# Kernel tuning notes

Hardware: AMD Instinct MI355X
Metric: run time of the kernel (lower is better)

## Reference

```python
import jax, jax.numpy as jnp
import numpy as np

ALPHA = 0.2
NEG = -9e15


def _gru(x, Wih, Whh, bih, bhh):
    # x: [B, T, F]; PyTorch nn.GRU cell equations, scan over time.
    H = Whh.shape[1]
    xg = jnp.einsum('btf,gf->btg', x, Wih) + bih  # [B,T,3H]

    def step(h, gi):
        gh = h @ Whh.T + bhh
        ir, iz, inn = jnp.split(gi, 3, axis=-1)
        hr, hz, hn = jnp.split(gh, 3, axis=-1)
        r = jax.nn.sigmoid(ir + hr)
        z = jax.nn.sigmoid(iz + hz)
        n = jnp.tanh(inn + r * hn)
        h = (1.0 - z) * n + z * h
        return h, h

    h0 = jnp.zeros((x.shape[0], H), x.dtype)
    _, ys = jax.lax.scan(step, h0, jnp.swapaxes(xg, 0, 1))
    return jnp.swapaxes(ys, 0, 1)  # [B,T,H]


def _gru_attn(x, Wih, Whh, bih, bhh, aw, ab):
    out = _gru(x, Wih, Whh, bih, bhh)              # [B,T,H]
    w = jax.nn.softmax(out @ aw + ab, axis=1)       # [B,T,1]
    return jnp.sum(out * w, axis=1)                 # [B,H]


def _gat(h, mask, W, a):
    # GraphAttentionLayer with concat=True: elu(softmax(mask(leakyrelu(Wh1+Wh2^T))) @ Wh)
    Wh = h @ W                                      # [N,O]
    O = W.shape[1]
    e = jax.nn.leaky_relu((Wh @ a[:O]) + (Wh @ a[O:]).T, ALPHA)  # [N,N]
    att = jax.nn.softmax(jnp.where(mask, e, NEG), axis=1)
    return jax.nn.elu(att @ Wh)


def setup_inputs() -> dict:
    key = jax.random.key(0)
    ks = iter(jax.random.split(key, 40))
    B, S, Wk, D, F = 1, 2048, 32, 5, 16
    H, E, NS = 128, 128, 16

    def rn(shape, scale=0.1):
        return jax.random.normal(next(ks), shape, jnp.float32) * scale

    inp = {
        'stock_features': jax.random.normal(next(ks), (B, S, Wk, D, F), jnp.float32),
        'stock_to_sector': jax.random.randint(next(ks), (S,), 0, NS, jnp.int32),
        'inter_adj': jax.random.randint(next(ks), (NS, NS), 0, 2, jnp.int32),
        'gru1_Wih': rn((3 * H, F)), 'gru1_Whh': rn((3 * H, H)),
        'gru1_bih': rn((3 * H,)), 'gru1_bhh': rn((3 * H,)),
        'attn1_w': rn((H, 1)), 'attn1_b': rn((1,)),
        'gat_intra_W': rn((H, E)), 'gat_intra_a': rn((2 * E, 1)),
        'grug_Wih': rn((3 * E, E)), 'grug_Whh': rn((3 * E, E)),
        'grug_bih': rn((3 * E,)), 'grug_bhh': rn((3 * E,)),
        'attng_w': rn((E, 1)), 'attng_b': rn((1,)),
        'grua_Wih': rn((3 * E, H)), 'grua_Whh': rn((3 * E, E)),
        'grua_bih': rn((3 * E,)), 'grua_bhh': rn((3 * E,)),
        'attna_w': rn((E, 1)), 'attna_b': rn((1,)),
        'gat_inter_W': rn((E, E)), 'gat_inter_a': rn((2 * E, 1)),
        'fusion_w': rn((3 * E, E)), 'fusion_b': rn((E,)),
        'ret_w': rn((E, 1)), 'ret_b': rn((1,)),
        'mov_w': rn((E, 1)), 'mov_b': rn((1,)),
    }
    return inp


def reference(stock_features, stock_to_sector, inter_adj,
              gru1_Wih, gru1_Whh, gru1_bih, gru1_bhh, attn1_w, attn1_b,
              gat_intra_W, gat_intra_a,
              grug_Wih, grug_Whh, grug_bih, grug_bhh, attng_w, attng_b,
              grua_Wih, grua_Whh, grua_bih, grua_bhh, attna_w, attna_b,
              gat_inter_W, gat_inter_a,
              fusion_w, fusion_b, ret_w, ret_b, mov_w, mov_b):
    B, S, Wk, D, F = stock_features.shape
    H = gru1_Whh.shape[1]
    E = gat_intra_W.shape[1]
    NS = inter_adj.shape[0]

    # Short-term: GRU-attention over days, vectorized over (batch, stock, week).
    x = stock_features.reshape(B * S * Wk, D, F)
    short = _gru_attn(x, gru1_Wih, gru1_Whh, gru1_bih, gru1_bhh, attn1_w, attn1_b)
    short = short.reshape(B, S, Wk, H)

    # Intra-sector GAT on last-week embeddings; per-sector softmax == block mask.
    same_sector = stock_to_sector[:, None] == stock_to_sector[None, :]  # [S,S]
    last = short[:, :, -1, :]                                            # [B,S,H]
    intra = jax.vmap(lambda h: _gat(h, same_sector, gat_intra_W, gat_intra_a))(last)  # [B,S,E]

    # Long-term GRU-attentions.
    lg = _gru_attn(intra.reshape(B * S, 1, E), grug_Wih, grug_Whh, grug_bih, grug_bhh,
                   attng_w, attng_b).reshape(B, S, E)
    la = _gru_attn(short.reshape(B * S, Wk, H), grua_Wih, grua_Whh, grua_bih, grua_bhh,
                   attna_w, attna_b).reshape(B, S, E)

    # Sector embeddings = mean of stock long-term embeddings per sector.
    def sector_mean(g):
        sums = jax.ops.segment_sum(g, stock_to_sector, num_segments=NS)
        cnt = jax.ops.segment_sum(jnp.ones((g.shape[0], 1), g.dtype),
                                  stock_to_sector, num_segments=NS)
        return sums / jnp.maximum(cnt, 1.0)

    sec = jax.vmap(sector_mean)(lg)                                      # [B,NS,E]
    imask = inter_adj > 0
    sec_out = jax.vmap(lambda h: _gat(h, imask, gat_inter_W, gat_inter_a))(sec)
    sec_ps = sec_out[:, stock_to_sector, :]                               # [B,S,E]

    fused = jnp.concatenate([lg, la, sec_ps], axis=-1) @ fusion_w + fusion_b
    returns = (fused @ ret_w + ret_b)[..., 0]
    moves = jax.nn.sigmoid(fused @ mov_w + mov_b)[..., 0]
    return jnp.stack([returns, moves])  # [2,B,S]
```

## Files before the change

### kernel.cpp

```cpp
#include <hip/hip_runtime.h>
#include <math.h>

#define LRELU_A 0.2f
#define NEGBIG (-9.0e15f)

typedef _Float16 f16;
typedef _Float16 f16x8 __attribute__((ext_vector_type(8)));
typedef _Float16 f16x4 __attribute__((ext_vector_type(4)));
typedef float floatx4 __attribute__((ext_vector_type(4)));

__device__ __forceinline__ float rcpf(float x){ return __builtin_amdgcn_rcpf(x); }
__device__ __forceinline__ float sigm(float x){ return rcpf(1.0f+__expf(-x)); }
__device__ __forceinline__ float gru_fuse(float xr, float xz, float xn_pre, float ghn, float h){
    float Er = __expf(-xr);
    float r  = rcpf(1.0f + Er);
    float En = __expf(2.0f*(xn_pre + r*ghn));
    float Ez = __expf(-xz);
    float Dn = En + 1.0f;
    float num = fmaf(h, Dn, (En - 1.0f)*Ez);
    float den = Dn * (1.0f + Ez);
    return num * rcpf(den);
}
__device__ __forceinline__ f16x8 load_cvt8(const float* __restrict__ p){
    float4 a = *(const float4*)p; float4 b = *(const float4*)(p+4);
    f16x8 r; r[0]=(f16)a.x; r[1]=(f16)a.y; r[2]=(f16)a.z; r[3]=(f16)a.w;
    r[4]=(f16)b.x; r[5]=(f16)b.y; r[6]=(f16)b.z; r[7]=(f16)b.w;
    return r;
}
#define MFMA16(A,B,C) __builtin_amdgcn_mfma_f32_16x16x32_f16((A),(B),(C),0,0,0)

__global__ __launch_bounds__(256) void prep_kernel(
    const float* __restrict__ g1Wih, const float* __restrict__ g1Whh,
    const float* __restrict__ gaWih, const float* __restrict__ gaWhh,
    const float* __restrict__ giW,   const float* __restrict__ fw,
    const float* __restrict__ geW,   const float* __restrict__ ggWih,
    const int* __restrict__ sec,
    f16* __restrict__ Wcat1, f16* __restrict__ WcatA,
    f16* __restrict__ WTp, f16* __restrict__ fwp, f16* __restrict__ gep,
    f16* __restrict__ ggp,
    int* __restrict__ memflat, int* __restrict__ pos,
    int* __restrict__ cnt, int* __restrict__ base)
{
    __shared__ int cs[16], wsc[16];
    const int b = blockIdx.x, tid = threadIdx.x;
    if (b < 160){
        for (int idx = b*256+tid; idx < 512*160; idx += 160*256){
            int r = idx/160, k = idx - r*160;
            float v = 0.0f;
            if (r < 256){ if (k < 32){ if (k < 16) v = g1Wih[r*16+k]; } else v = g1Whh[r*128 + (k-32)]; }
            else if (r < 384){ if (k < 16) v = g1Wih[r*16+k]; }
            else { if (k >= 32) v = g1Whh[(r-128)*128 + (k-32)]; }
            Wcat1[idx] = (f16)v;
        }
    } else if (b < 416){
        for (int idx = (b-160)*256+tid; idx < 512*256; idx += 256*256){
            int r = idx >> 8, k = idx & 255;
            float v = 0.0f;
            if (r < 256){ v = (k < 128) ? gaWih[r*128+k] : gaWhh[r*128 + (k-128)]; }
            else if (r < 384){ if (k < 128) v = gaWih[r*128+k]; }
            else { if (k >= 128) v = gaWhh[(r-128)*128 + (k-128)]; }
            WcatA[idx] = (f16)v;
        }
    } else if (b < 480){
        int idx = (b-416)*256+tid;
        int e=idx&7, lane=(idx>>3)&63, fr=idx>>9;
        int kb=fr&3, jb=fr>>2;
        int k = kb*32 + (lane>>4)*8 + e, col = jb*16 + (lane&15);
        WTp[idx] = (f16)giW[k*128 + col];
    } else if (b < 672){
        int idx = (b-480)*256+tid;
        int e=idx&7, lane=(idx>>3)&63, fr=idx>>9;
        int kb=fr%12, jb=fr/12;
        int k = kb*32 + (lane>>4)*8 + e, col = jb*16 + (lane&15);
        fwp[idx] = (f16)fw[k*128 + col];
    } else if (b < 736){
        int idx = (b-672)*256+tid;
        int e=idx&7, lane=(idx>>3)&63, fr=idx>>9;
        int kb=fr&3, jb=fr>>2;
        int k = kb*32 + (lane>>4)*8 + e, col = jb*16 + (lane&15);
        gep[idx] = (f16)geW[k*128 + col];
    } else if (b < 928){
        int idx = (b-736)*256+tid;
        int e=idx&7, lane=(idx>>3)&63, fr=idx>>9;
        int kb=fr&3, jb=(fr>>2)&7, G=fr>>5;
        int row = G*128 + jb*16 + (lane&15), k = kb*32 + (lane>>4)*8 + e;
        ggp[idx] = (f16)ggWih[row*128 + k];
    } else {
        if (tid < 16) cs[tid] = 0;
        __syncthreads();
        for (int s = tid; s < 2048; s += 256) atomicAdd(&cs[sec[s]], 1);
        __syncthreads();
        if (tid == 0){
            int acc = 0;
            for (int g=0; g<16; g++){ cnt[g]=cs[g]; base[g]=acc; wsc[g]=acc; acc+=cs[g]; }
        }
        __syncthreads();
        for (int s = tid; s < 2048; s += 256){
            int g = sec[s];
            int p = atomicAdd(&wsc[g], 1);
            memflat[p] = s;
            pos[s] = p;
        }
    }
}

__global__ __launch_bounds__(512,2) void gru_short(
    const float* __restrict__ x, const f16* __restrict__ Wcat,
    const float* __restrict__ bih, const float* __restrict__ bhh,
    const float* __restrict__ aw, const float* __restrict__ ab,
    f16* __restrict__ out)
{
    __shared__ __align__(16) f16 xs[5][32][40];
    __shared__ __align__(16) f16 hs[2][32][136];
    __shared__ float scpart[2][8][32];
    const int tid = threadIdx.x, w = tid>>6, lane = tid&63;
    const int c = lane&15, quad = lane>>4;

    { f16x4 z4 = {0,0,0,0};
      f16x4* zx = (f16x4*)&xs[0][0][0];
      for (int i=tid; i<1600; i+=512) zx[i] = z4; }

    const int jrow = w*16 + c;
    f16x8 Ar[5], Az[5], Agi, Agh[4];
#pragma unroll
    for (int kb=0;kb<5;kb++){
        Ar[kb] = *(const f16x8*)&Wcat[(size_t)(jrow)*160 + kb*32 + quad*8];
        Az[kb] = *(const f16x8*)&Wcat[(size_t)(128+jrow)*160 + kb*32 + quad*8];
    }
    Agi = *(const f16x8*)&Wcat[(size_t)(256+jrow)*160 + quad*8];
#pragma unroll
    for (int i=0;i<4;i++)
        Agh[i] = *(const f16x8*)&Wcat[(size_t)(384+jrow)*160 + 32 + i*32 + quad*8];

    float brz_r[4], brz_z[4], b_in[4], b_hn[4], awr[4];
#pragma unroll
    for (int r=0;r<4;r++){
        int j = w*16 + quad*4 + r;
        brz_r[r] = bih[j] + bhh[j];
        brz_z[r] = bih[128+j] + bhh[128+j];
        b_in[r] = bih[256+j]; b_hn[r] = bhh[256+j];
        awr[r] = aw[j];
    }
    const float abv = ab[0];

    const int s0i = tid/20,        q0 = tid - 20*s0i;
    const int i1  = tid + 512;
    const int s1i = i1/20,         q1 = i1 - 20*s1i;
    const bool pf1 = (tid < 128);
    float4 xpf0, xpf1;
    {
        const size_t base0 = (size_t)(blockIdx.x*8)*32;
        xpf0 = *(const float4*)&x[(base0 + s0i)*80 + q0*4];
        if (pf1) xpf1 = *(const float4*)&x[(base0 + s1i)*80 + q1*4];
    }

#pragma unroll 1
    for (int tile=0; tile<8; ++tile){
        const int s0 = (blockIdx.x*8 + tile)*32;
        { f16x4 z4 = {0,0,0,0};
          f16x4* zh = (f16x4*)&hs[1][0][0];
          for (int i=tid; i<1088; i+=512) zh[i] = z4; }
        {
            int t = (q0*4)>>4, f = (q0*4)&15;
            f16x4 h4; h4[0]=(f16)xpf0.x; h4[1]=(f16)xpf0.y; h4[2]=(f16)xpf0.z; h4[3]=(f16)xpf0.w;
            *(f16x4*)&xs[t][s0i][f] = h4;
            if (pf1){
                int t1 = (q1*4)>>4, f1 = (q1*4)&15;
                f16x4 g4; g4[0]=(f16)xpf1.x; g4[1]=(f16)xpf1.y; g4[2]=(f16)xpf1.z; g4[3]=(f16)xpf1.w;
                *(f16x4*)&xs[t1][s1i][f1] = g4;
            }
        }
        if (tile < 7){
            const size_t basen = (size_t)(s0 + 32);
            xpf0 = *(const float4*)&x[(basen + s0i)*80 + q0*4];
            if (pf1) xpf1 = *(const float4*)&x[(basen + s1i)*80 + q1*4];
        }
        float hreg[2][4], aacc[2][4], l_[2] = {0.0f, 0.0f};
#pragma unroll
        for (int st=0; st<2; st++)
#pragma unroll
            for (int r=0;r<4;r++){ hreg[st][r]=0.0f; aacc[st][r]=0.0f; }
        __syncthreads();

#pragma unroll 1
        for (int t=0; t<5; ++t){
            const int rp = (t&1)^1, wp = t&1;
            f16x8 Bx[2], Bh[2][4];
#pragma unroll
            for (int st=0; st<2; st++){
                Bx[st] = *(const f16x8*)&xs[t][st*16+c][quad*8];
#pragma unroll
                for (int i=0;i<4;i++)
                    Bh[st][i] = *(const f16x8*)&hs[rp][st*16+c][i*32+quad*8];
            }
            if (t > 0){
#pragma unroll
                for (int st=0; st<2; st++){
                    float sc = abv;
#pragma unroll
                    for (int ww=0; ww<8; ww++) sc += scpart[rp][ww][st*16+c];
                    float e = __expf(sc);
                    l_[st] += e;
#pragma unroll
                    for (int r=0;r<4;r++) aacc[st][r] += e*hreg[st][r];
                }
            }
            float sp[2];
#pragma unroll
            for (int st=0; st<2; st++){
                floatx4 ar = {0,0,0,0}, az = {0,0,0,0}, agi = {0,0,0,0}, agh = {0,0,0,0};
                ar = MFMA16(Ar[0], Bx[st], ar);
                az = MFMA16(Az[0], Bx[st], az);
                agi = MFMA16(Agi, Bx[st], agi);
#pragma unroll
                for (int i=0;i<4;i++){
                    ar = MFMA16(Ar[1+i], Bh[st][i], ar);
                    az = MFMA16(Az[1+i], Bh[st][i], az);
                    agh = MFMA16(Agh[i], Bh[st][i], agh);
                }
                f16x4 h4;
                sp[st] = 0.0f;
#pragma unroll
                for (int r=0;r<4;r++){
                    float hn = gru_fuse(ar[r] + brz_r[r], az[r] + brz_z[r],
                                        agi[r] + b_in[r], agh[r] + b_hn[r], hreg[st][r]);
                    hreg[st][r] = hn; h4[r] = (f16)hn;
                    sp[st] += hn * awr[r];
                }
                *(f16x4*)&hs[wp][st*16 + c][w*16 + quad*4] = h4;
            }
#pragma unroll
            for (int st=0; st<2; st++){
                sp[st] += __shfl_xor(sp[st], 16);
                sp[st] += __shfl_xor(sp[st], 32);
            }
            if (lane < 16){ scpart[wp][w][lane] = sp[0]; scpart[wp][w][16+lane] = sp[1]; }
            __syncthreads();
        }
#pragma unroll
        for (int st=0; st<2; st++){
            float sc = abv;
#pragma unroll
            for (int ww=0; ww<8; ww++) sc += scpart[0][ww][st*16+c];
            float e = __expf(sc);
            l_[st] += e;
            float inv = rcpf(l_[st]);
            f16x4 h4;
#pragma unroll
            for (int r=0;r<4;r++) h4[r] = (f16)((aacc[st][r] + e*hreg[st][r])*inv);
            *(f16x4*)&hs[0][st*16 + c][w*16 + quad*4] = h4;
        }
        __syncthreads();
        { int s = tid>>4, p = tid&15;
          *(f16x8*)&out[(size_t)(s0+s)*128 + p*8] = *(const f16x8*)&hs[0][s][p*8]; }
    }
}

__global__ __launch_bounds__(512,2) void gru_la_gatprep(
    const f16* __restrict__ xseq, const f16* __restrict__ Wcat,
    const float* __restrict__ bih, const float* __restrict__ bhh,
    const float* __restrict__ aw, const float* __restrict__ ab,
    f16* __restrict__ out,
    const f16* __restrict__ WTp, const float* __restrict__ gia,
    const int* __restrict__ memflat,
    f16* __restrict__ Whs, float* __restrict__ ers, float* __restrict__ el)
{
    __shared__ __align__(16) f16 xs[2][16][136];
    __shared__ __align__(16) f16 hs[2][16][136];
    __shared__ float scpart[2][8][16];
    __shared__ __align__(16) float tbuf[32][132];
    __shared__ int rows[32];
    const int tid = threadIdx.x, w = tid>>6, lane = tid&63;
    const int c = lane&15, quad = lane>>4;

    if (blockIdx.x >= 256){
        const int p0 = (blockIdx.x-256)*32;
        if (tid < 32) rows[tid] = memflat[p0 + tid];
        __syncthreads();
        f16x8 A[2][4];
#pragma unroll
        for (int mt=0;mt<2;mt++)
#pragma unroll
            for (int kb=0;kb<4;kb++)
                A[mt][kb] = *(const f16x8*)&xseq[((size_t)rows[mt*16+c]*32 + 31)*128 + kb*32 + quad*8];
        {
            f16x8 B[4];
#pragma unroll
            for (int kb=0;kb<4;kb++)
                B[kb] = *(const f16x8*)&WTp[(((size_t)(w*4+kb))*64 + lane)*8];
            floatx4 acc[2] = {{0,0,0,0},{0,0,0,0}};
#pragma unroll
            for (int kb=0;kb<4;kb++){
                acc[0] = MFMA16(A[0][kb], B[kb], acc[0]);
                acc[1] = MFMA16(A[1][kb], B[kb], acc[1]);
            }
#pragma unroll
            for (int mt=0;mt<2;mt++)
#pragma unroll
                for (int r=0;r<4;r++)
                    tbuf[mt*16 + quad*4 + r][w*16 + c] = acc[mt][r];
        }
        __syncthreads();
        for (int i=tid; i<1024; i+=512){
            int s = i>>5, p = i&31;
            float4 v = *(const float4*)&tbuf[s][p*4];
            f16x4 h4; h4[0]=(f16)v.x; h4[1]=(f16)v.y; h4[2]=(f16)v.z; h4[3]=(f16)v.w;
            *(f16x4*)&Whs[(size_t)(p0+s)*128 + p*4] = h4;
        }
        for (int k=0; k<4; k++){
            int row = w*4 + k;
            float w0 = tbuf[row][lane], w1 = tbuf[row][64+lane];
            float v1 = w0*gia[lane]     + w1*gia[64+lane];
            float v2 = w0*gia[128+lane] + w1*gia[192+lane];
#pragma unroll
            for (int off=32; off; off>>=1){ v1 += __shfl_down(v1,off); v2 += __shfl_down(v2,off); }
            if (lane==0){ el[rows[row]] = v1; ers[p0+row] = v2; }
        }
        return;
    }
    const int s0 = blockIdx.x*8;
    { f16x4 z4 = {0,0,0,0};
      f16x4* za = (f16x4*)&xs[0][0][0];
      for (int i=tid; i<1088; i+=512) za[i] = z4;
      f16x4* zh = (f16x4*)&hs[0][0][0];
      for (int i=tid; i<1088; i+=512) zh[i] = z4; }
    __syncthreads();
    if (tid < 128){
        int s = tid>>4, p = tid&15;
        *(f16x8*)&xs[0][s][p*8] = *(const f16x8*)&xseq[((size_t)(s0+s)*32 + 0)*128 + p*8];
    }
    const int jrow = w*16 + c;
    f16x8 Ar[8], Az[8], Agi[4], Agh[4];
#pragma unroll
    for (int kb=0;kb<8;kb++){
        Ar[kb] = *(const f16x8*)&Wcat[(size_t)(jrow)*256 + kb*32 + quad*8];
        Az[kb] = *(const f16x8*)&Wcat[(size_t)(128+jrow)*256 + kb*32 + quad*8];
    }
#pragma unroll
    for (int i=0;i<4;i++){
        Agi[i] = *(const f16x8*)&Wcat[(size_t)(256+jrow)*256 + i*32 + quad*8];
        Agh[i] = *(const f16x8*)&Wcat[(size_t)(384+jrow)*256 + 128 + i*32 + quad*8];
    }
    float brz_r[4], brz_z[4], b_in[4], b_hn[4], awr[4];
#pragma unroll
    for (int r=0;r<4;r++){
        int j = w*16 + quad*4 + r;
        brz_r[r] = bih[j] + bhh[j];
        brz_z[r] = bih[128+j] + bhh[128+j];
        b_in[r] = bih[256+j]; b_hn[r] = bhh[256+j];
        awr[r] = aw[j];
    }
    const float abv = ab[0];
    float hreg[4] = {0,0,0,0}, aacc[4] = {0,0,0,0}, l_ = 0.0f;
    __syncthreads();

#pragma unroll 1
    for (int t=0; t<32; ++t){
        const int rp = (t&1)^1, wp = t&1, xp = t&1;
        f16x8 Bx[4], Bh[4];
#pragma unroll
        for (int i=0;i<4;i++){
            Bx[i] = *(const f16x8*)&xs[xp][c][i*32+quad*8];
            Bh[i] = *(const f16x8*)&hs[rp][c][i*32+quad*8];
        }
        f16x8 xstage;
        const bool do_stage = (t < 31) && (tid < 128);
        if (do_stage){
            int s = tid>>4, p = tid&15;
            xstage = *(const f16x8*)&xseq[((size_t)(s0+s)*32 + t+1)*128 + p*8];
        }
        if (t > 0){
            float sc = abv;
#pragma unroll
            for (int ww=0; ww<8; ww++) sc += scpart[rp][ww][c];
            float e = __expf(sc);
            l_ += e;
#pragma unroll
            for (int r=0;r<4;r++) aacc[r] += e*hreg[r];
        }
        floatx4 ar = {0,0,0,0}, az = {0,0,0,0}, agi = {0,0,0,0}, agh = {0,0,0,0};
#pragma unroll
        for (int i=0;i<4;i++){
            ar = MFMA16(Ar[i], Bx[i], ar);
            az = MFMA16(Az[i], Bx[i], az);
            agi = MFMA16(Agi[i], Bx[i], agi);
        }
#pragma unroll
        for (int i=0;i<4;i++){
            ar = MFMA16(Ar[4+i], Bh[i], ar);
            az = MFMA16(Az[4+i], Bh[i], az);
            agh = MFMA16(Agh[i], Bh[i], agh);
        }
        f16x4 h4;
        float sp = 0.0f;
#pragma unroll
        for (int r=0;r<4;r++){
            float hn = gru_fuse(ar[r] + brz_r[r], az[r] + brz_z[r],
                                agi[r] + b_in[r], agh[r] + b_hn[r], hreg[r]);
            hreg[r] = hn; h4[r] = (f16)hn;
            sp += hn * awr[r];
        }
        *(f16x4*)&hs[wp][c][w*16 + quad*4] = h4;
        if (do_stage){
            int s = tid>>4, p = tid&15;
            *(f16x8*)&xs[xp^1][s][p*8] = xstage;
        }
        sp += __shfl_xor(sp, 16);
        sp += __shfl_xor(sp, 32);
        if (lane < 16) scpart[wp][w][lane] = sp;
        __syncthreads();
    }
    {
        float sc = abv;
#pragma unroll
        for (int ww=0; ww<8; ww++) sc += scpart[1][ww][c];
        float e = __expf(sc);
        l_ += e;
        float inv = rcpf(l_);
        f16x4 h4;
#pragma unroll
        for (int r=0;r<4;r++) h4[r] = (f16)((aacc[r] + e*hreg[r])*inv);
        *(f16x4*)&hs[1][c][w*16 + quad*4] = h4;
    }
    __syncthreads();
    if (tid < 128){
        int s = tid>>4, p = tid&15;
        *(f16x8*)&out[(size_t)(s0+s)*128 + p*8] = *(const f16x8*)&hs[1][s][p*8];
    }
}

__global__ __launch_bounds__(256) void gat_intra_mem_kernel(
    const f16* __restrict__ Whs, const float* __restrict__ ers,
    const float* __restrict__ el, const int* __restrict__ sec,
    const int* __restrict__ cnt, const int* __restrict__ base,
    f16* __restrict__ outp, int S)
{
    int wave = threadIdx.x>>6, lane = threadIdx.x&63;
    int i = blockIdx.x*4 + wave;
    if (i>=S) return;
    int g = sec[i];
    int n = cnt[g], b = base[g];
    float eli = el[i];
    float m = -INFINITY;
    for (int jj=lane; jj<n; jj+=64){
        float v = eli + ers[b+jj]; v = v>0.f? v : LRELU_A*v;
        m = fmaxf(m, v);
    }
#pragma unroll
    for (int off=32; off; off>>=1) m = fmaxf(m, __shfl_xor(m, off));
    float l = 0.f, c0=0.f, c1=0.f;
#pragma unroll 4
    for (int jj=0; jj<n; jj++){
        float v = eli + ers[b+jj]; v = v>0.f? v : LRELU_A*v;
        float p = __expf(v-m);
        l += p;
        c0 += p*(float)Whs[(size_t)(b+jj)*128 + lane];
        c1 += p*(float)Whs[(size_t)(b+jj)*128 + 64 + lane];
    }
    float il = rcpf(l);
    c0 *= il; c1 *= il;
    outp[(size_t)i*128+lane]    = (f16)(c0>0.f? c0 : expm1f(c0));
    outp[(size_t)i*128+64+lane] = (f16)(c1>0.f? c1 : expm1f(c1));
}

__global__ __launch_bounds__(256) void lg_mfma(
    const f16* __restrict__ intra16, const f16* __restrict__ ggp,
    const float* __restrict__ bih, const float* __restrict__ bhh,
    const int* __restrict__ pos,
    f16* __restrict__ lgout, f16* __restrict__ lgs)
{
    __shared__ __align__(16) f16 tbuf[32][136];
    const int tid = threadIdx.x, w = tid>>6, lane = tid&63;
    const int c = lane&15, quad = lane>>4;
    const int s0 = blockIdx.x*32;
    f16x8 A[2][4];
#pragma unroll
    for (int mt=0;mt<2;mt++)
#pragma unroll
        for (int kb=0;kb<4;kb++)
            A[mt][kb] = *(const f16x8*)&intra16[(size_t)(s0+mt*16+c)*128 + kb*32 + quad*8];
#pragma unroll
    for (int i=0;i<2;i++){
        int jb = w*2 + i;
        int j = jb*16 + c;
        f16x8 Br[4], Bz[4], Bn[4];
#pragma unroll
        for (int kb=0;kb<4;kb++){
            Br[kb] = *(const f16x8*)&ggp[(((size_t)((0*8+jb)*4+kb))*64 + lane)*8];
            Bz[kb] = *(const f16x8*)&ggp[(((size_t)((1*8+jb)*4+kb))*64 + lane)*8];
            Bn[kb] = *(const f16x8*)&ggp[(((size_t)((2*8+jb)*4+kb))*64 + lane)*8];
        }
        float b_r = bih[j] + bhh[j];
        float b_z = bih[128+j] + bhh[128+j];
        float b_i = bih[256+j], b_h = bhh[256+j];
        floatx4 ar[2] = {{0,0,0,0},{0,0,0,0}};
        floatx4 az[2] = {{0,0,0,0},{0,0,0,0}};
        floatx4 an[2] = {{0,0,0,0},{0,0,0,0}};
#pragma unroll
        for (int kb=0;kb<4;kb++)
#pragma unroll
            for (int mt=0;mt<2;mt++){
                ar[mt] = MFMA16(A[mt][kb], Br[kb], ar[mt]);
                az[mt] = MFMA16(A[mt][kb], Bz[kb], az[mt]);
                an[mt] = MFMA16(A[mt][kb], Bn[kb], an[mt]);
            }
#pragma unroll
        for (int mt=0;mt<2;mt++)
#pragma unroll
            for (int r=0;r<4;r++){
                float Er = __expf(-(ar[mt][r] + b_r));
                float rg = rcpf(1.0f + Er);
                float En = __expf(2.0f*(an[mt][r] + b_i + rg*b_h));
                float Ez = __expf(-(az[mt][r] + b_z));
                float v = (En - 1.0f)*Ez * rcpf((En + 1.0f)*(1.0f + Ez));
                tbuf[mt*16 + quad*4 + r][j] = (f16)v;
            }
    }
    __syncthreads();
    for (int i=tid; i<512; i+=256){
        int s = i>>4, p = i&15;
        f16x8 v = *(const f16x8*)&tbuf[s][p*8];
        *(f16x8*)&lgout[(size_t)(s0+s)*128 + p*8] = v;
        *(f16x8*)&lgs[(size_t)pos[s0+s]*128 + p*8] = v;
    }
}

__global__ __launch_bounds__(1024) void gat_inter_fused(
    const f16* __restrict__ lgs, const int* __restrict__ cnt,
    const int* __restrict__ base, const int* __restrict__ adj,
    const f16* __restrict__ gep, const float* __restrict__ a,
    float* __restrict__ outp)
{
    __shared__ __align__(16) float hs[16][132];
    __shared__ __align__(16) float Whs[16][132];
    __shared__ float el[16], er[16];
    __shared__ float att[16][16];
    const int tid = threadIdx.x, w = tid>>6, lane = tid&63;
    const int c = lane&15, quad = lane>>4;

    {
        int n = cnt[w], b = base[w];
        const int rowoff = lane>>4;
        const int colb = (lane&15)*8;
        float acc[8] = {0,0,0,0,0,0,0,0};
        for (int r = rowoff; r < n; r += 4){
            f16x8 v = *(const f16x8*)&lgs[(size_t)(b+r)*128 + colb];
#pragma unroll
            for (int k=0;k<8;k++) acc[k] += (float)v[k];
        }
#pragma unroll
        for (int k=0;k<8;k++){
            acc[k] += __shfl_xor(acc[k], 16);
            acc[k] += __shfl_xor(acc[k], 32);
        }
        if (lane < 16){
            float inv = rcpf(fmaxf((float)n, 1.0f));
#pragma unroll
            for (int k=0;k<8;k++) hs[w][colb+k] = acc[k]*inv;
        }
    }
    __syncthreads();
    if (w < 8){
        f16x8 A[4], B[4];
#pragma unroll
        for (int kb=0;kb<4;kb++){
            A[kb] = load_cvt8(&hs[c][kb*32 + quad*8]);
            B[kb] = *(const f16x8*)&gep[(((size_t)(w*4+kb))*64 + lane)*8];
        }
        floatx4 acc = {0,0,0,0};
#pragma unroll
        for (int kb=0;kb<4;kb++) acc = MFMA16(A[kb], B[kb], acc);
#pragma unroll
        for (int r=0;r<4;r++) Whs[quad*4 + r][w*16 + c] = acc[r];
    }
    __syncthreads();
    {
        int half = lane>>5, l = lane&31;
        const float* av = a + half*128;
        float acc2 = 0.f;
#pragma unroll
        for (int k=0;k<4;k++) acc2 += Whs[w][l+32*k]*av[l+32*k];
#pragma unroll
        for (int off=1; off<32; off<<=1) acc2 += __shfl_xor(acc2, off);
        if (l==0){ if (half) er[w]=acc2; else el[w]=acc2; }
    }
    __syncthreads();
    if (tid<16){
        int i=tid; float m=NEGBIG; float e[16];
        for(int j=0;j<16;j++){
            float v = el[i]+er[j]; v = v>0.f? v : LRELU_A*v;
            e[j] = (adj[i*16+j]>0)? v : NEGBIG;
            m = fmaxf(m,e[j]);
        }
        float l=0.f;
        for(int j=0;j<16;j++){ float p=__expf(e[j]-m); att[i][j]=p; l+=p; }
        float il = rcpf(l);
        for(int j=0;j<16;j++) att[i][j] *= il;
    }
    __syncthreads();
#pragma unroll
    for (int i=0;i<2;i++){
        int idx=i*1024+tid; int o=idx&127, s=idx>>7;
        float acc=0.f;
#pragma unroll
        for(int j=0;j<16;j++) acc += att[s][j]*Whs[j][o];
        outp[s*128+o] = acc>0.f? acc : expm1f(acc);
    }
}

__global__ __launch_bounds__(256) void fused_mfma(
    const f16* __restrict__ lg16, const f16* __restrict__ la16,
    const float* __restrict__ seco, const int* __restrict__ sec,
    const f16* __restrict__ fwp,
    const float* __restrict__ fb, const float* __restrict__ rw,
    const float* __restrict__ rb, const float* __restrict__ mw,
    const float* __restrict__ mb, float* __restrict__ outp)
{
    __shared__ float rpart[4][32], mpart[4][32];
    const int tid = threadIdx.x, w = tid>>6, lane = tid&63;
    const int c = lane&15, quad = lane>>4;
    const int s0 = blockIdx.x*32;
    f16x8 A[2][12];
#pragma unroll
    for (int mt=0;mt<2;mt++){
        int row = s0 + mt*16 + c;
        int g = sec[row];
#pragma unroll
        for (int kb=0;kb<4;kb++){
            A[mt][kb]   = *(const f16x8*)&lg16[(size_t)row*128 + kb*32 + quad*8];
            A[mt][4+kb] = *(const f16x8*)&la16[(size_t)row*128 + kb*32 + quad*8];
            A[mt][8+kb] = load_cvt8(&seco[(size_t)g*128 + kb*32 + quad*8]);
        }
    }
    float rsum[2][4] = {{0,0,0,0},{0,0,0,0}};
    float msum[2][4] = {{0,0,0,0},{0,0,0,0}};
#pragma unroll
    for (int i=0;i<2;i++){
        int jb = w*2 + i;
        int col = jb*16 + c;
        f16x8 B[12];
#pragma unroll
        for (int kb=0;kb<12;kb++)
            B[kb] = *(const f16x8*)&fwp[(((size_t)(jb*12+kb))*64 + lane)*8];
        floatx4 acc[2] = {{0,0,0,0},{0,0,0,0}};
#pragma unroll
        for (int kb=0;kb<12;kb++){
            acc[0] = MFMA16(A[0][kb], B[kb], acc[0]);
            acc[1] = MFMA16(A[1][kb], B[kb], acc[1]);
        }
        float fbv = fb[col], rwv = rw[col], mwv = mw[col];
#pragma unroll
        for (int mt=0;mt<2;mt++)
#pragma unroll
            for (int r=0;r<4;r++){
                float fu = acc[mt][r] + fbv;
                rsum[mt][r] += fu*rwv;
                msum[mt][r] += fu*mwv;
            }
    }
#pragma unroll
    for (int mt=0;mt<2;mt++)
#pragma unroll
        for (int r=0;r<4;r++){
#pragma unroll
            for (int off=1; off<16; off<<=1){
                rsum[mt][r] += __shfl_xor(rsum[mt][r], off);
                msum[mt][r] += __shfl_xor(msum[mt][r], off);
            }
            if (c==0){
                rpart[w][mt*16 + quad*4 + r] = rsum[mt][r];
                mpart[w][mt*16 + quad*4 + r] = msum[mt][r];
            }
        }
    __syncthreads();
    if (tid < 32){
        int s = tid;
        float rs = rb[0], ms = mb[0];
#pragma unroll
        for (int ww=0; ww<4; ww++){ rs += rpart[ww][s]; ms += mpart[ww][s]; }
        outp[s0+s] = rs;
        outp[2048 + s0 + s] = sigm(ms);
    }
}

extern "C" void kernel_launch(void* const* d_in, const int* in_sizes, int n_in,
                              void* d_out, int out_size, void* d_ws, size_t ws_size,
                              hipStream_t stream) {
    const float* sf    = (const float*)d_in[0];
    const int*   sec   = (const int*)  d_in[1];
    const int*   adj   = (const int*)  d_in[2];
    const float* g1Wih = (const float*)d_in[3];
    const float* g1Whh = (const float*)d_in[4];
    const float* g1bih = (const float*)d_in[5];
    const float* g1bhh = (const float*)d_in[6];
    const float* a1w   = (const float*)d_in[7];
    const float* a1b   = (const float*)d_in[8];
    const float* giW   = (const float*)d_in[9];
    const float* gia   = (const float*)d_in[10];
    const float* ggWih = (const float*)d_in[11];
    const float* ggbih = (const float*)d_in[13];
    const float* ggbhh = (const float*)d_in[14];
    const float* gaWih = (const float*)d_in[17];
    const float* gaWhh = (const float*)d_in[18];
    const float* gabih = (const float*)d_in[19];
    const float* gabhh = (const float*)d_in[20];
    const float* aaw   = (const float*)d_in[21];
    const float* aab   = (const float*)d_in[22];
    const float* geW   = (const float*)d_in[23];
    const float* gea   = (const float*)d_in[24];
    const float* fw    = (const float*)d_in[25];
    const float* fb    = (const float*)d_in[26];
    const float* rw    = (const float*)d_in[27];
    const float* rb    = (const float*)d_in[28];
    const float* mw    = (const float*)d_in[29];
    const float* mb    = (const float*)d_in[30];

    char* p = (char*)d_ws;
    f16*   shrt16 = (f16*)p;   p += (size_t)65536*128*2;
    f16*   intra16= (f16*)p;   p += (size_t)262144*2;
    f16*   lg16   = (f16*)p;   p += (size_t)262144*2;
    f16*   la16   = (f16*)p;   p += (size_t)262144*2;
    f16*   Whs    = (f16*)p;   p += (size_t)262144*2;
    f16*   lgs    = (f16*)p;   p += (size_t)262144*2;
    f16*   Wcat1  = (f16*)p;   p += (size_t)512*160*2;
    f16*   WcatA  = (f16*)p;   p += (size_t)512*256*2;
    f16*   WTp    = (f16*)p;   p += (size_t)16384*2;
    f16*   gep    = (f16*)p;   p += (size_t)16384*2;
    f16*   fwp    = (f16*)p;   p += (size_t)49152*2;
    f16*   ggp    = (f16*)p;   p += (size_t)49152*2;
    float* el     = (float*)p; p += 2048*4;
    float* ers    = (float*)p; p += 2048*4;
    float* seco   = (float*)p; p += 2048*4;
    int*   memflat= (int*)p;   p += 2048*4;
    int*   pos    = (int*)p;   p += 2048*4;
    int*   cnt    = (int*)p;   p += 16*4;
    int*   basep  = (int*)p;   p += 16*4;

    prep_kernel<<<929,256,0,stream>>>(g1Wih, g1Whh, gaWih, gaWhh, giW, fw, geW, ggWih, sec,
                                      Wcat1, WcatA, WTp, fwp, gep, ggp,
                                      memflat, pos, cnt, basep);
    gru_short<<<256,512,0,stream>>>(sf, Wcat1, g1bih, g1bhh, a1w, a1b, shrt16);
    gru_la_gatprep<<<320,512,0,stream>>>(shrt16, WcatA, gabih, gabhh, aaw, aab, la16,
                                         WTp, gia, memflat, Whs, ers, el);
    gat_intra_mem_kernel<<<512,256,0,stream>>>(Whs, ers, el, sec, cnt, basep, intra16, 2048);
    lg_mfma<<<64,256,0,stream>>>(intra16, ggp, ggbih, ggbhh, pos, lg16, lgs);
    gat_inter_fused<<<1,1024,0,stream>>>(lgs, cnt, basep, adj, gep, gea, seco);
    fused_mfma<<<64,256,0,stream>>>(lg16, la16, seco, sec, fwp, fb, rw, rb, mw, mb, (float*)d_out);
}
```

Before: 285.3 us.

## Precompute next-step input-gate MFMAs one step ahead with triple-buffered x staging

In the attention-GRU kernel, the input-projection MFMAs for step t+1 are now computed during step t. They are carried in registers, so the serial recurrence critical path only contains the hidden-state MFMAs. The x staging buffer goes from double to triple buffering, and loads are prefetched two steps ahead. The cost is more accumulator registers and LDS, which may hurt occupancy under the 512x2 launch bound.

```diff
diff --git a/kernel.cpp b/kernel.cpp
--- a/kernel.cpp
+++ b/kernel.cpp
@@ -265,7 +265,7 @@
     const int* __restrict__ memflat,
     f16* __restrict__ Whs, float* __restrict__ ers, float* __restrict__ el)
 {
-    __shared__ __align__(16) f16 xs[2][16][136];
+    __shared__ __align__(16) f16 xs[3][16][136];
     __shared__ __align__(16) f16 hs[2][16][136];
     __shared__ float scpart[2][8][16];
     __shared__ __align__(16) float tbuf[32][132];
@@ -321,13 +321,14 @@
     const int s0 = blockIdx.x*8;
     { f16x4 z4 = {0,0,0,0};
       f16x4* za = (f16x4*)&xs[0][0][0];
-      for (int i=tid; i<1088; i+=512) za[i] = z4;
+      for (int i=tid; i<1632; i+=512) za[i] = z4;
       f16x4* zh = (f16x4*)&hs[0][0][0];
       for (int i=tid; i<1088; i+=512) zh[i] = z4; }
     __syncthreads();
-    if (tid < 128){
-        int s = tid>>4, p = tid&15;
-        *(f16x8*)&xs[0][s][p*8] = *(const f16x8*)&xseq[((size_t)(s0+s)*32 + 0)*128 + p*8];
+    if (tid < 256){
+        int half = tid>>7, r = tid&127;
+        int s = r>>4, p = r&15;
+        *(f16x8*)&xs[half][s][p*8] = *(const f16x8*)&xseq[((size_t)(s0+s)*32 + half)*128 + p*8];
     }
     const int jrow = w*16 + c;
     f16x8 Ar[8], Az[8], Agi[4], Agh[4];
@@ -354,20 +355,45 @@
     float hreg[4] = {0,0,0,0}, aacc[4] = {0,0,0,0}, l_ = 0.0f;
     __syncthreads();
 
+    floatx4 xar = {0,0,0,0}, xaz = {0,0,0,0}, xagi = {0,0,0,0};
+    {
+        f16x8 Bx0[4];
+#pragma unroll
+        for (int i=0;i<4;i++) Bx0[i] = *(const f16x8*)&xs[0][c][i*32+quad*8];
+#pragma unroll
+        for (int i=0;i<4;i++){
+            xar  = MFMA16(Ar[i],  Bx0[i], xar);
+            xaz  = MFMA16(Az[i],  Bx0[i], xaz);
+            xagi = MFMA16(Agi[i], Bx0[i], xagi);
+        }
+    }
+
 #pragma unroll 1
     for (int t=0; t<32; ++t){
-        const int rp = (t&1)^1, wp = t&1, xp = t&1;
-        f16x8 Bx[4], Bh[4];
-#pragma unroll
-        for (int i=0;i<4;i++){
-            Bx[i] = *(const f16x8*)&xs[xp][c][i*32+quad*8];
+        const int rp = (t&1)^1, wp = t&1;
+        f16x8 Bh[4];
+#pragma unroll
+        for (int i=0;i<4;i++)
             Bh[i] = *(const f16x8*)&hs[rp][c][i*32+quad*8];
+        floatx4 nar = {0,0,0,0}, naz = {0,0,0,0}, nagi = {0,0,0,0};
+        if (t < 31){
+            const f16* xb = &xs[(t+1)%3][0][0];
+            f16x8 Bxn[4];
+#pragma unroll
+            for (int i=0;i<4;i++)
+                Bxn[i] = *(const f16x8*)&xb[(size_t)c*136 + i*32 + quad*8];
+#pragma unroll
+            for (int i=0;i<4;i++){
+                nar  = MFMA16(Ar[i],  Bxn[i], nar);
+                naz  = MFMA16(Az[i],  Bxn[i], naz);
+                nagi = MFMA16(Agi[i], Bxn[i], nagi);
+            }
         }
         f16x8 xstage;
-        const bool do_stage = (t < 31) && (tid < 128);
+        const bool do_stage = (t < 30) && (tid < 128);
         if (do_stage){
             int s = tid>>4, p = tid&15;
-            xstage = *(const f16x8*)&xseq[((size_t)(s0+s)*32 + t+1)*128 + p*8];
+            xstage = *(const f16x8*)&xseq[((size_t)(s0+s)*32 + t+2)*128 + p*8];
         }
         if (t > 0){
             float sc = abv;
@@ -378,37 +404,32 @@
 #pragma unroll
             for (int r=0;r<4;r++) aacc[r] += e*hreg[r];
         }
-        floatx4 ar = {0,0,0,0}, az = {0,0,0,0}, agi = {0,0,0,0}, agh = {0,0,0,0};
+        floatx4 ar = xar, az = xaz, agh = {0,0,0,0};
 #pragma unroll
         for (int i=0;i<4;i++){
-            ar = MFMA16(Ar[i], Bx[i], ar);
-            az = MFMA16(Az[i], Bx[i], az);
-            agi = MFMA16(Agi[i], Bx[i], agi);
-        }
-#pragma unroll
-        for (int i=0;i<4;i++){
-            ar = MFMA16(Ar[4+i], Bh[i], ar);
-            az = MFMA16(Az[4+i], Bh[i], az);
-            agh = MFMA16(Agh[i], Bh[i], agh);
+            ar  = MFMA16(Ar[4+i], Bh[i], ar);
+            az  = MFMA16(Az[4+i], Bh[i], az);
+            agh = MFMA16(Agh[i],  Bh[i], agh);
         }
         f16x4 h4;
         float sp = 0.0f;
 #pragma unroll
         for (int r=0;r<4;r++){
             float hn = gru_fuse(ar[r] + brz_r[r], az[r] + brz_z[r],
-                                agi[r] + b_in[r], agh[r] + b_hn[r], hreg[r]);
+                                xagi[r] + b_in[r], agh[r] + b_hn[r], hreg[r]);
             hreg[r] = hn; h4[r] = (f16)hn;
             sp += hn * awr[r];
         }
         *(f16x4*)&hs[wp][c][w*16 + quad*4] = h4;
         if (do_stage){
             int s = tid>>4, p = tid&15;
-            *(f16x8*)&xs[xp^1][s][p*8] = xstage;
+            *(f16x8*)&xs[(t+2)%3][s][p*8] = xstage;
         }
         sp += __shfl_xor(sp, 16);
         sp += __shfl_xor(sp, 32);
         if (lane < 16) scpart[wp][w][lane] = sp;
         __syncthreads();
+        xar = nar; xaz = naz; xagi = nagi;
     }
     {
         float sc = abv;
```

After: 287.5 us. No clear change (+0.8%).
